# Kernel tuning notes

Hardware: AMD Instinct MI355X
Metric: run time of the kernel (lower is better)

The kernel has to match this reference:

```python
import jax, jax.numpy as jnp
import numpy as np


def setup_inputs() -> dict:
    key = jax.random.key(0)
    k_x, k_q, k_k, k_v = jax.random.split(key, 4)
    B, S, D = 8, 1024, 768
    H, DH = 12, 64
    scale = 1.0 / np.sqrt(D)
    return {
        "x": jax.random.normal(k_x, (B, S, D), dtype=jnp.float32),
        "Wq": jax.random.normal(k_q, (H, D, DH), dtype=jnp.float32) * scale,
        "Wk": jax.random.normal(k_k, (H, D, DH), dtype=jnp.float32) * scale,
        "Wv": jax.random.normal(k_v, (H, D, DH), dtype=jnp.float32) * scale,
    }


def reference(x, Wq, Wk, Wv):
    # x: [B, S, D]; Wq/Wk/Wv: [H, D, DH] (per-head Linear weights, no bias)
    B, S, D = x.shape
    H, _, DH = Wq.shape
    q = jnp.einsum("bsd,hde->bhse", x, Wq)  # [B,H,S,DH]
    k = jnp.einsum("bsd,hde->bhse", x, Wk)
    v = jnp.einsum("bsd,hde->bhse", x, Wv)
    scores = jnp.einsum("bhse,bhte->bhst", q, k) / jnp.sqrt(jnp.float32(DH))
    causal = jnp.tril(jnp.ones((S, S), dtype=bool))  # keep lower triangle
    scores = jnp.where(causal, scores, -jnp.inf)
    attn = jax.nn.softmax(scores, axis=-1)  # dropout = 0.0 -> identity
    ctx = jnp.einsum("bhst,bhte->bhse", attn, v)  # [B,H,S,DH]
    # concat heads on last dim: [B,S,H*DH]
    return ctx.transpose(0, 2, 1, 3).reshape(B, S, H * DH)
```

## Files before the change

### kernel.cpp

```cpp
#include <hip/hip_runtime.h>


#define Bq 8
#define Sq 1024
#define Dq 768
#define Hq 12
#define DHq 64

typedef _Float16 f16;
typedef f16 f16x8 __attribute__((ext_vector_type(8)));
typedef float f32x4 __attribute__((ext_vector_type(4)));

#define MFMA16(a, b, c) __builtin_amdgcn_mfma_f32_16x16x32_f16(a, b, c, 0, 0, 0)

#define QSCL 0.1803368801111244f

#if __has_builtin(__builtin_amdgcn_exp2f)
#define EXP2(x) __builtin_amdgcn_exp2f(x)
#else
#define EXP2(x) exp2f(x)
#endif

__device__ __forceinline__ void gload16(const f16* g, f16* l) {
  __builtin_amdgcn_global_load_lds(
      (const __attribute__((address_space(1))) void*)g,
      (__attribute__((address_space(3))) void*)l, 16, 0, 0);
}

__global__ __launch_bounds__(256) void cvt_x_kernel(const float* __restrict__ x,
                                                    f16* __restrict__ xh) {
  int i = blockIdx.x * 256 + threadIdx.x;
  const float4* src = reinterpret_cast<const float4*>(x) + i * 2;
  float4 a = src[0], b = src[1];
  f16x8 o;
  o[0] = (f16)a.x; o[1] = (f16)a.y; o[2] = (f16)a.z; o[3] = (f16)a.w;
  o[4] = (f16)b.x; o[5] = (f16)b.y; o[6] = (f16)b.z; o[7] = (f16)b.w;
  *reinterpret_cast<f16x8*>(xh + i * 8) = o;
}

__global__ __launch_bounds__(256) void cvt_w_kernel(const float* __restrict__ Wq,
                                                    const float* __restrict__ Wk,
                                                    const float* __restrict__ Wv,
                                                    f16* __restrict__ WT) {
  __shared__ float tile[64][65];
  const int kt = blockIdx.x, h = blockIdx.y, w = blockIdx.z;
  const float* W = (w == 0) ? Wq : (w == 1) ? Wk : Wv;
  const int t = threadIdx.x;
  const int c0 = t & 63, r4 = t >> 6;
#pragma unroll
  for (int i = 0; i < 16; i++) {
    int kr = i * 4 + r4;
    tile[kr][c0] = W[((size_t)h * Dq + kt * 64 + kr) * DHq + c0];
  }
  __syncthreads();
#pragma unroll
  for (int i = 0; i < 16; i++) {
    int e2 = i * 4 + r4;
    WT[((size_t)(w * Hq + h) * DHq + e2) * Dq + kt * 64 + c0] = (f16)tile[c0][e2];
  }
}

__global__ __launch_bounds__(256) void proj_kernel(const f16* __restrict__ xh,
                                                   const f16* __restrict__ WT,
                                                   f16* __restrict__ Q,
                                                   f16* __restrict__ K,
                                                   f16* __restrict__ Vt) {
  __shared__ __align__(1024) f16 smem[30720];

  const int mt = blockIdx.x;
  const int h = blockIdx.y;
  const int row0 = mt * 128;
  const int t = threadIdx.x;
  const int wv = t >> 6;
  const int lane = t & 63;
  const int g = lane >> 4;
  const int ql = lane & 15;
  const int wvm = wv >> 1, wvn = wv & 1;

  const int lr = lane >> 2;
  const int scg = (lane & 3) ^ ((lane >> 3) & 3);

  const f16* xsrc = xh + (size_t)row0 * Dq;
  const f16* wsrc = WT + (size_t)h * DHq * Dq;

  const f16* gA0 = xsrc + (size_t)(wv * 32 + lr) * Dq + scg * 8;
  const f16* gA1 = gA0 + (size_t)16 * Dq;
  const int n0 = wv * 48 + lr, n1 = n0 + 16, n2 = n0 + 32;
  const f16* gB0 = wsrc + ((size_t)(n0 >> 6) * Hq * DHq + (n0 & 63)) * Dq + scg * 8;
  const f16* gB1 = wsrc + ((size_t)(n1 >> 6) * Hq * DHq + (n1 & 63)) * Dq + scg * 8;
  const f16* gB2 = wsrc + ((size_t)(n2 >> 6) * Hq * DHq + (n2 & 63)) * Dq + scg * 8;

  f32x4 acc[4][6] = {};

#define PROJ_STAGE(buf)                                              \
  do {                                                               \
    f16* sA_ = smem + (buf) * 4096 + wv * 1024;                      \
    f16* sB_ = smem + 12288 + (buf) * 6144 + wv * 1536;              \
    gload16(gA0, sA_); gload16(gA1, sA_ + 512);                      \
    gload16(gB0, sB_); gload16(gB1, sB_ + 512);                      \
    gload16(gB2, sB_ + 1024);                                        \
    gA0 += 32; gA1 += 32; gB0 += 32; gB1 += 32; gB2 += 32;           \
  } while (0)

  PROJ_STAGE(0);
  PROJ_STAGE(1);

  const int rq = (g ^ ((ql >> 1) & 3)) * 8;
  const f16* rA = smem + (wvm * 64 + ql) * 32 + rq;
  const f16* rB = smem + 12288 + (wvn * 96 + ql) * 32 + rq;

#pragma unroll
  for (int step = 0; step < 24; step++) {
    if (step < 23) asm volatile("s_waitcnt vmcnt(5) lgkmcnt(0)" ::: "memory");
    else           asm volatile("s_waitcnt vmcnt(0) lgkmcnt(0)" ::: "memory");
    __builtin_amdgcn_s_barrier();
    __builtin_amdgcn_sched_barrier(0);
    if (step < 22) PROJ_STAGE((step + 2) % 3);
    const int cur = step % 3;
    f16x8 af[4], bf[6];
#pragma unroll
    for (int mf = 0; mf < 4; mf++)
      af[mf] = *reinterpret_cast<const f16x8*>(rA + cur * 4096 + mf * 512);
#pragma unroll
    for (int nf = 0; nf < 6; nf++)
      bf[nf] = *reinterpret_cast<const f16x8*>(rB + cur * 6144 + nf * 512);
    __builtin_amdgcn_s_setprio(1);
#pragma unroll
    for (int mf = 0; mf < 4; mf++)
#pragma unroll
      for (int nf = 0; nf < 6; nf++)
        acc[mf][nf] = MFMA16(af[mf], bf[nf], acc[mf][nf]);
    __builtin_amdgcn_s_setprio(0);
  }
#undef PROJ_STAGE
  __syncthreads();

  const int b = row0 >> 10;
  const int s0 = row0 & 1023;
  const size_t base_sd = ((size_t)(b * Hq + h) * Sq) * DHq;

#pragma unroll
  for (int nf = 0; nf < 6; nf++) {
    const int c = wvn * 96 + nf * 16 + ql;
    const int w = c >> 6;
    if (w < 2) {
      f16* dst = (w == 0 ? Q : K);
      const float scl = (w == 0) ? QSCL : 1.0f;
      const int e = c & 63;
#pragma unroll
      for (int mf = 0; mf < 4; mf++) {
        const int sr = wvm * 64 + mf * 16 + g * 4;
#pragma unroll
        for (int r = 0; r < 4; r++)
          dst[base_sd + (size_t)(s0 + sr + r) * DHq + e] = (f16)(acc[mf][nf][r] * scl);
      }
    }
  }

  f16* vbuf = smem;
#pragma unroll
  for (int nf = 2; nf < 6; nf++) {
    if (wvn == 1) {
      const int e = (96 + nf * 16 + ql) & 63;
#pragma unroll
      for (int mf = 0; mf < 4; mf++) {
        const int sr = wvm * 64 + mf * 16 + g * 4;
        union { f16 hh[4]; uint2 u; } z;
#pragma unroll
        for (int r = 0; r < 4; r++) z.hh[r] = (f16)acc[mf][nf][r];
        *reinterpret_cast<uint2*>(&vbuf[e * 136 + sr]) = z.u;
      }
    }
  }
  __syncthreads();
#pragma unroll
  for (int i = 0; i < 4; i++) {
    int c = t + 256 * i;
    int e = c >> 4, p = (c & 15) * 8;
    *reinterpret_cast<uint4*>(Vt + base_sd + (size_t)e * Sq + s0 + p) =
        *reinterpret_cast<const uint4*>(vbuf + e * 136 + p);
  }
}

__global__ __launch_bounds__(256) void attn_kernel(const f16* __restrict__ Q,
                                                   const f16* __restrict__ K,
                                                   const f16* __restrict__ Vt,
                                                   float* __restrict__ out) {
  __shared__ __align__(16) f16 k_lds[2][64][72];
  __shared__ __align__(16) f16 vt_lds[2][64][72];

  const int L = blockIdx.x;
  const int m = L >> 3;
  const int pr = m / Hq;
  const int bh = (L & 7) * Hq + (m % Hq);
  const int t = threadIdx.x;
  const int wv = t >> 6;
  const int lane = t & 63;
  const int g = lane >> 4;
  const int ql = lane & 15;

  const f16* Qb = Q + (size_t)bh * Sq * DHq;
  const f16* Kb = K + (size_t)bh * Sq * DHq;
  const f16* Vtb = Vt + (size_t)bh * DHq * Sq;
  const int b = bh / Hq, h = bh % Hq;

  const int r0 = t >> 3;
  const int p0 = (t & 7) * 8;

  for (int ph = 0; ph < 2; ph++) {
    const int mt = ph ? (15 - pr) : pr;
    const int q0 = mt * 64;
    const int qg = q0 + wv * 16 + ql;
    f16x8 qf0 = *reinterpret_cast<const f16x8*>(Qb + (size_t)qg * DHq + g * 8);
    f16x8 qf1 = *reinterpret_cast<const f16x8*>(Qb + (size_t)qg * DHq + 32 + g * 8);

    f32x4 o_acc[4] = {};
    float m_r = -__builtin_inff(), l_r = 0.f;

    uint4 kreg0, kreg1, vreg0, vreg1;
    kreg0 = *reinterpret_cast<const uint4*>(Kb + (size_t)r0 * DHq + p0);
    kreg1 = *reinterpret_cast<const uint4*>(Kb + (size_t)(32 + r0) * DHq + p0);
    vreg0 = *reinterpret_cast<const uint4*>(Vtb + (size_t)r0 * Sq + p0);
    vreg1 = *reinterpret_cast<const uint4*>(Vtb + (size_t)(32 + r0) * Sq + p0);
    *reinterpret_cast<uint4*>(&k_lds[0][r0][p0]) = kreg0;
    *reinterpret_cast<uint4*>(&k_lds[0][32 + r0][p0]) = kreg1;
    *reinterpret_cast<uint4*>(&vt_lds[0][r0][p0]) = vreg0;
    *reinterpret_cast<uint4*>(&vt_lds[0][32 + r0][p0]) = vreg1;
    if (mt >= 1) {
      kreg0 = *reinterpret_cast<const uint4*>(Kb + (size_t)(64 + r0) * DHq + p0);
      kreg1 = *reinterpret_cast<const uint4*>(Kb + (size_t)(96 + r0) * DHq + p0);
      vreg0 = *reinterpret_cast<const uint4*>(Vtb + (size_t)r0 * Sq + 64 + p0);
      vreg1 = *reinterpret_cast<const uint4*>(Vtb + (size_t)(32 + r0) * Sq + 64 + p0);
    }
    __syncthreads();

    int cur = 0;
    for (int kt = 0; kt <= mt; kt++) {
      f32x4 sf[4] = {};
      __builtin_amdgcn_s_setprio(1);
#pragma unroll
      for (int nt = 0; nt < 4; nt++) {
        f16x8 kf0 = *reinterpret_cast<const f16x8*>(&k_lds[cur][nt * 16 + ql][g * 8]);
        f16x8 kf1 = *reinterpret_cast<const f16x8*>(&k_lds[cur][nt * 16 + ql][32 + g * 8]);
        sf[nt] = MFMA16(kf0, qf0, sf[nt]);
        sf[nt] = MFMA16(kf1, qf1, sf[nt]);
      }
      __builtin_amdgcn_s_setprio(0);

      if (kt == mt) {
#pragma unroll
        for (int nt = 0; nt < 4; nt++)
#pragma unroll
          for (int r = 0; r < 4; r++)
            if (nt * 16 + g * 4 + r > wv * 16 + ql) sf[nt][r] = -__builtin_inff();
      }

      float rowmax = sf[0][0];
#pragma unroll
      for (int nt = 0; nt < 4; nt++)
#pragma unroll
        for (int r = 0; r < 4; r++) rowmax = fmaxf(rowmax, sf[nt][r]);
      rowmax = fmaxf(rowmax, __shfl_xor(rowmax, 16, 64));
      rowmax = fmaxf(rowmax, __shfl_xor(rowmax, 32, 64));
      float mnew = fmaxf(m_r, rowmax);
      float corr = EXP2(m_r - mnew);
      float p[4][4];
      float rs = 0.f;
#pragma unroll
      for (int nt = 0; nt < 4; nt++)
#pragma unroll
        for (int r = 0; r < 4; r++) {
          float pe = EXP2(sf[nt][r] - mnew);
          p[nt][r] = pe;
          rs += pe;
        }
      rs += __shfl_xor(rs, 16, 64);
      rs += __shfl_xor(rs, 32, 64);
      l_r = l_r * corr + rs;
      m_r = mnew;
#pragma unroll
      for (int nt = 0; nt < 4; nt++) {
        o_acc[nt][0] *= corr; o_acc[nt][1] *= corr;
        o_acc[nt][2] *= corr; o_acc[nt][3] *= corr;
      }

      uint32_t pk[4][2];
#pragma unroll
      for (int nt = 0; nt < 4; nt++) {
        union { f16 hh[2]; uint32_t u; } z0, z1;
        z0.hh[0] = (f16)p[nt][0]; z0.hh[1] = (f16)p[nt][1];
        z1.hh[0] = (f16)p[nt][2]; z1.hh[1] = (f16)p[nt][3];
        pk[nt][0] = z0.u; pk[nt][1] = z1.u;
      }
      const int srcA = ((g & 1) * 2) * 16 + ql;
      const int srcB = srcA + 16;
      const bool selhi = (g >> 1) != 0;
      f16x8 pf[2];
#pragma unroll
      for (int ks = 0; ks < 2; ks++) {
        uint32_t aA0 = (uint32_t)__shfl((int)pk[2 * ks][0], srcA, 64);
        uint32_t aA1 = (uint32_t)__shfl((int)pk[2 * ks][1], srcA, 64);
        uint32_t aB0 = (uint32_t)__shfl((int)pk[2 * ks][0], srcB, 64);
        uint32_t aB1 = (uint32_t)__shfl((int)pk[2 * ks][1], srcB, 64);
        uint32_t bA0 = (uint32_t)__shfl((int)pk[2 * ks + 1][0], srcA, 64);
        uint32_t bA1 = (uint32_t)__shfl((int)pk[2 * ks + 1][1], srcA, 64);
        uint32_t bB0 = (uint32_t)__shfl((int)pk[2 * ks + 1][0], srcB, 64);
        uint32_t bB1 = (uint32_t)__shfl((int)pk[2 * ks + 1][1], srcB, 64);
        union { uint32_t w[4]; f16x8 v; } z;
        z.w[0] = selhi ? bA0 : aA0;
        z.w[1] = selhi ? bA1 : aA1;
        z.w[2] = selhi ? bB0 : aB0;
        z.w[3] = selhi ? bB1 : aB1;
        pf[ks] = z.v;
      }

      __builtin_amdgcn_s_setprio(1);
#pragma unroll
      for (int nt = 0; nt < 4; nt++) {
        f16x8 vf0 = *reinterpret_cast<const f16x8*>(&vt_lds[cur][nt * 16 + ql][g * 8]);
        f16x8 vf1 = *reinterpret_cast<const f16x8*>(&vt_lds[cur][nt * 16 + ql][32 + g * 8]);
        o_acc[nt] = MFMA16(vf0, pf[0], o_acc[nt]);
        o_acc[nt] = MFMA16(vf1, pf[1], o_acc[nt]);
      }
      __builtin_amdgcn_s_setprio(0);

      if (kt < mt) {
        *reinterpret_cast<uint4*>(&k_lds[cur ^ 1][r0][p0]) = kreg0;
        *reinterpret_cast<uint4*>(&k_lds[cur ^ 1][32 + r0][p0]) = kreg1;
        *reinterpret_cast<uint4*>(&vt_lds[cur ^ 1][r0][p0]) = vreg0;
        *reinterpret_cast<uint4*>(&vt_lds[cur ^ 1][32 + r0][p0]) = vreg1;
        if (kt + 2 <= mt) {
          const int kv0 = (kt + 2) * 64;
          kreg0 = *reinterpret_cast<const uint4*>(Kb + (size_t)(kv0 + r0) * DHq + p0);
          kreg1 = *reinterpret_cast<const uint4*>(Kb + (size_t)(kv0 + 32 + r0) * DHq + p0);
          vreg0 = *reinterpret_cast<const uint4*>(Vtb + (size_t)r0 * Sq + kv0 + p0);
          vreg1 = *reinterpret_cast<const uint4*>(Vtb + (size_t)(32 + r0) * Sq + kv0 + p0);
        }
      }
      __syncthreads();
      cur ^= 1;
    }

    float rl = 1.0f / l_r;
    float* op = out + ((size_t)(b * Sq + qg)) * (Hq * DHq) + h * DHq;
#pragma unroll
    for (int nt = 0; nt < 4; nt++) {
      float4 st = { o_acc[nt][0] * rl, o_acc[nt][1] * rl,
                    o_acc[nt][2] * rl, o_acc[nt][3] * rl };
      *reinterpret_cast<float4*>(op + nt * 16 + g * 4) = st;
    }
  }
}

extern "C" void kernel_launch(void* const* d_in, const int* in_sizes, int n_in,
                              void* d_out, int out_size, void* d_ws, size_t ws_size,
                              hipStream_t stream) {
  const float* x = (const float*)d_in[0];
  const float* Wq = (const float*)d_in[1];
  const float* Wk = (const float*)d_in[2];
  const float* Wv = (const float*)d_in[3];
  float* out = (float*)d_out;

  const size_t off_xb = 0;
  const size_t off_wt = 12582912;
  const size_t off_q = 16121856;
  const size_t off_k = 28704768;
  const size_t off_v = 41287680;
  const size_t need = 53870592;
  if (ws_size < need) return;

  char* ws = (char*)d_ws;
  f16* xh = (f16*)(ws + off_xb);
  f16* WT = (f16*)(ws + off_wt);
  f16* Qd = (f16*)(ws + off_q);
  f16* Kd = (f16*)(ws + off_k);
  f16* Vtd = (f16*)(ws + off_v);

  cvt_x_kernel<<<3072, 256, 0, stream>>>(x, xh);
  cvt_w_kernel<<<dim3(12, 12, 3), 256, 0, stream>>>(Wq, Wk, Wv, WT);
  proj_kernel<<<dim3(64, 12), 256, 0, stream>>>(xh, WT, Qd, Kd, Vtd);
  attn_kernel<<<768, 256, 0, stream>>>(Qd, Kd, Vtd, out);
}
```

Measured before the change: 85.03 us.

## Launch one block per query tile, longest-first, with lazy softmax rescaling

The attention kernel previously had each block process a pair of complementary causal query tiles in sequence. It now launches twice as many blocks, each handling one query tile, ordered so the longest tiles are dispatched first. Online softmax now skips the max update and accumulator rescale when the new row max stays within 8 (log2 units) of the running max, and the max and sum reductions use tree form. This adds parallelism and removes serial rescale work, at the cost of more block launches and reloading Q/K per block. Skipping rescales lets exponentials reach up to 2^8, which stays within fp16 range.

```diff
diff --git a/kernel.cpp b/kernel.cpp
--- a/kernel.cpp
+++ b/kernel.cpp
@@ -190,9 +190,9 @@
   __shared__ __align__(16) f16 vt_lds[2][64][72];
 
   const int L = blockIdx.x;
-  const int m = L >> 3;
-  const int pr = m / Hq;
-  const int bh = (L & 7) * Hq + (m % Hq);
+  const int i = L >> 3;
+  const int bh = (L & 7) * Hq + (i % Hq);
+  const int mt = 15 - (i / Hq);
   const int t = threadIdx.x;
   const int wv = t >> 6;
   const int lane = t & 63;
@@ -207,148 +207,150 @@
   const int r0 = t >> 3;
   const int p0 = (t & 7) * 8;
 
-  for (int ph = 0; ph < 2; ph++) {
-    const int mt = ph ? (15 - pr) : pr;
-    const int q0 = mt * 64;
-    const int qg = q0 + wv * 16 + ql;
-    f16x8 qf0 = *reinterpret_cast<const f16x8*>(Qb + (size_t)qg * DHq + g * 8);
-    f16x8 qf1 = *reinterpret_cast<const f16x8*>(Qb + (size_t)qg * DHq + 32 + g * 8);
-
-    f32x4 o_acc[4] = {};
-    float m_r = -__builtin_inff(), l_r = 0.f;
-
-    uint4 kreg0, kreg1, vreg0, vreg1;
-    kreg0 = *reinterpret_cast<const uint4*>(Kb + (size_t)r0 * DHq + p0);
-    kreg1 = *reinterpret_cast<const uint4*>(Kb + (size_t)(32 + r0) * DHq + p0);
-    vreg0 = *reinterpret_cast<const uint4*>(Vtb + (size_t)r0 * Sq + p0);
-    vreg1 = *reinterpret_cast<const uint4*>(Vtb + (size_t)(32 + r0) * Sq + p0);
-    *reinterpret_cast<uint4*>(&k_lds[0][r0][p0]) = kreg0;
-    *reinterpret_cast<uint4*>(&k_lds[0][32 + r0][p0]) = kreg1;
-    *reinterpret_cast<uint4*>(&vt_lds[0][r0][p0]) = vreg0;
-    *reinterpret_cast<uint4*>(&vt_lds[0][32 + r0][p0]) = vreg1;
-    if (mt >= 1) {
-      kreg0 = *reinterpret_cast<const uint4*>(Kb + (size_t)(64 + r0) * DHq + p0);
-      kreg1 = *reinterpret_cast<const uint4*>(Kb + (size_t)(96 + r0) * DHq + p0);
-      vreg0 = *reinterpret_cast<const uint4*>(Vtb + (size_t)r0 * Sq + 64 + p0);
-      vreg1 = *reinterpret_cast<const uint4*>(Vtb + (size_t)(32 + r0) * Sq + 64 + p0);
-    }
-    __syncthreads();
-
-    int cur = 0;
-    for (int kt = 0; kt <= mt; kt++) {
-      f32x4 sf[4] = {};
-      __builtin_amdgcn_s_setprio(1);
-#pragma unroll
-      for (int nt = 0; nt < 4; nt++) {
-        f16x8 kf0 = *reinterpret_cast<const f16x8*>(&k_lds[cur][nt * 16 + ql][g * 8]);
-        f16x8 kf1 = *reinterpret_cast<const f16x8*>(&k_lds[cur][nt * 16 + ql][32 + g * 8]);
-        sf[nt] = MFMA16(kf0, qf0, sf[nt]);
-        sf[nt] = MFMA16(kf1, qf1, sf[nt]);
-      }
-      __builtin_amdgcn_s_setprio(0);
-
-      if (kt == mt) {
-#pragma unroll
-        for (int nt = 0; nt < 4; nt++)
-#pragma unroll
-          for (int r = 0; r < 4; r++)
-            if (nt * 16 + g * 4 + r > wv * 16 + ql) sf[nt][r] = -__builtin_inff();
-      }
-
-      float rowmax = sf[0][0];
+  const int q0 = mt * 64;
+  const int qg = q0 + wv * 16 + ql;
+  f16x8 qf0 = *reinterpret_cast<const f16x8*>(Qb + (size_t)qg * DHq + g * 8);
+  f16x8 qf1 = *reinterpret_cast<const f16x8*>(Qb + (size_t)qg * DHq + 32 + g * 8);
+
+  f32x4 o_acc[4] = {};
+  float m_r = -__builtin_inff(), l_r = 0.f;
+
+  uint4 kreg0, kreg1, vreg0, vreg1;
+  kreg0 = *reinterpret_cast<const uint4*>(Kb + (size_t)r0 * DHq + p0);
+  kreg1 = *reinterpret_cast<const uint4*>(Kb + (size_t)(32 + r0) * DHq + p0);
+  vreg0 = *reinterpret_cast<const uint4*>(Vtb + (size_t)r0 * Sq + p0);
+  vreg1 = *reinterpret_cast<const uint4*>(Vtb + (size_t)(32 + r0) * Sq + p0);
+  *reinterpret_cast<uint4*>(&k_lds[0][r0][p0]) = kreg0;
+  *reinterpret_cast<uint4*>(&k_lds[0][32 + r0][p0]) = kreg1;
+  *reinterpret_cast<uint4*>(&vt_lds[0][r0][p0]) = vreg0;
+  *reinterpret_cast<uint4*>(&vt_lds[0][32 + r0][p0]) = vreg1;
+  if (mt >= 1) {
+    kreg0 = *reinterpret_cast<const uint4*>(Kb + (size_t)(64 + r0) * DHq + p0);
+    kreg1 = *reinterpret_cast<const uint4*>(Kb + (size_t)(96 + r0) * DHq + p0);
+    vreg0 = *reinterpret_cast<const uint4*>(Vtb + (size_t)r0 * Sq + 64 + p0);
+    vreg1 = *reinterpret_cast<const uint4*>(Vtb + (size_t)(32 + r0) * Sq + 64 + p0);
+  }
+  __syncthreads();
+
+  int cur = 0;
+  for (int kt = 0; kt <= mt; kt++) {
+    f32x4 sf[4] = {};
+    __builtin_amdgcn_s_setprio(1);
+#pragma unroll
+    for (int nt = 0; nt < 4; nt++) {
+      f16x8 kf0 = *reinterpret_cast<const f16x8*>(&k_lds[cur][nt * 16 + ql][g * 8]);
+      f16x8 kf1 = *reinterpret_cast<const f16x8*>(&k_lds[cur][nt * 16 + ql][32 + g * 8]);
+      sf[nt] = MFMA16(kf0, qf0, sf[nt]);
+      sf[nt] = MFMA16(kf1, qf1, sf[nt]);
+    }
+    __builtin_amdgcn_s_setprio(0);
+
+    if (kt == mt) {
 #pragma unroll
       for (int nt = 0; nt < 4; nt++)
 #pragma unroll
-        for (int r = 0; r < 4; r++) rowmax = fmaxf(rowmax, sf[nt][r]);
-      rowmax = fmaxf(rowmax, __shfl_xor(rowmax, 16, 64));
-      rowmax = fmaxf(rowmax, __shfl_xor(rowmax, 32, 64));
+        for (int r = 0; r < 4; r++)
+          if (nt * 16 + g * 4 + r > wv * 16 + ql) sf[nt][r] = -__builtin_inff();
+    }
+
+    float t0 = fmaxf(fmaxf(sf[0][0], sf[0][1]), fmaxf(sf[0][2], sf[0][3]));
+    float t1 = fmaxf(fmaxf(sf[1][0], sf[1][1]), fmaxf(sf[1][2], sf[1][3]));
+    float t2 = fmaxf(fmaxf(sf[2][0], sf[2][1]), fmaxf(sf[2][2], sf[2][3]));
+    float t3 = fmaxf(fmaxf(sf[3][0], sf[3][1]), fmaxf(sf[3][2], sf[3][3]));
+    float rowmax = fmaxf(fmaxf(t0, t1), fmaxf(t2, t3));
+    rowmax = fmaxf(rowmax, __shfl_xor(rowmax, 16, 64));
+    rowmax = fmaxf(rowmax, __shfl_xor(rowmax, 32, 64));
+
+    if (!__all(rowmax <= m_r + 8.f)) {
       float mnew = fmaxf(m_r, rowmax);
       float corr = EXP2(m_r - mnew);
-      float p[4][4];
-      float rs = 0.f;
-#pragma unroll
-      for (int nt = 0; nt < 4; nt++)
-#pragma unroll
-        for (int r = 0; r < 4; r++) {
-          float pe = EXP2(sf[nt][r] - mnew);
-          p[nt][r] = pe;
-          rs += pe;
-        }
-      rs += __shfl_xor(rs, 16, 64);
-      rs += __shfl_xor(rs, 32, 64);
-      l_r = l_r * corr + rs;
-      m_r = mnew;
+      l_r *= corr;
 #pragma unroll
       for (int nt = 0; nt < 4; nt++) {
         o_acc[nt][0] *= corr; o_acc[nt][1] *= corr;
         o_acc[nt][2] *= corr; o_acc[nt][3] *= corr;
       }
-
-      uint32_t pk[4][2];
-#pragma unroll
-      for (int nt = 0; nt < 4; nt++) {
-        union { f16 hh[2]; uint32_t u; } z0, z1;
-        z0.hh[0] = (f16)p[nt][0]; z0.hh[1] = (f16)p[nt][1];
-        z1.hh[0] = (f16)p[nt][2]; z1.hh[1] = (f16)p[nt][3];
-        pk[nt][0] = z0.u; pk[nt][1] = z1.u;
+      m_r = mnew;
+    }
+
+    float p[4][4];
+#pragma unroll
+    for (int nt = 0; nt < 4; nt++)
+#pragma unroll
+      for (int r = 0; r < 4; r++) p[nt][r] = EXP2(sf[nt][r] - m_r);
+    float s0 = (p[0][0] + p[0][1]) + (p[0][2] + p[0][3]);
+    float s1 = (p[1][0] + p[1][1]) + (p[1][2] + p[1][3]);
+    float s2 = (p[2][0] + p[2][1]) + (p[2][2] + p[2][3]);
+    float s3 = (p[3][0] + p[3][1]) + (p[3][2] + p[3][3]);
+    float rs = (s0 + s1) + (s2 + s3);
+    rs += __shfl_xor(rs, 16, 64);
+    rs += __shfl_xor(rs, 32, 64);
+    l_r += rs;
+
+    uint32_t pk[4][2];
+#pragma unroll
+    for (int nt = 0; nt < 4; nt++) {
+      union { f16 hh[2]; uint32_t u; } z0, z1;
+      z0.hh[0] = (f16)p[nt][0]; z0.hh[1] = (f16)p[nt][1];
+      z1.hh[0] = (f16)p[nt][2]; z1.hh[1] = (f16)p[nt][3];
+      pk[nt][0] = z0.u; pk[nt][1] = z1.u;
+    }
+    const int srcA = ((g & 1) * 2) * 16 + ql;
+    const int srcB = srcA + 16;
+    const bool selhi = (g >> 1) != 0;
+    f16x8 pf[2];
+#pragma unroll
+    for (int ks = 0; ks < 2; ks++) {
+      uint32_t aA0 = (uint32_t)__shfl((int)pk[2 * ks][0], srcA, 64);
+      uint32_t aA1 = (uint32_t)__shfl((int)pk[2 * ks][1], srcA, 64);
+      uint32_t aB0 = (uint32_t)__shfl((int)pk[2 * ks][0], srcB, 64);
+      uint32_t aB1 = (uint32_t)__shfl((int)pk[2 * ks][1], srcB, 64);
+      uint32_t bA0 = (uint32_t)__shfl((int)pk[2 * ks + 1][0], srcA, 64);
+      uint32_t bA1 = (uint32_t)__shfl((int)pk[2 * ks + 1][1], srcA, 64);
+      uint32_t bB0 = (uint32_t)__shfl((int)pk[2 * ks + 1][0], srcB, 64);
+      uint32_t bB1 = (uint32_t)__shfl((int)pk[2 * ks + 1][1], srcB, 64);
+      union { uint32_t w[4]; f16x8 v; } z;
+      z.w[0] = selhi ? bA0 : aA0;
+      z.w[1] = selhi ? bA1 : aA1;
+      z.w[2] = selhi ? bB0 : aB0;
+      z.w[3] = selhi ? bB1 : aB1;
+      pf[ks] = z.v;
+    }
+
+    __builtin_amdgcn_s_setprio(1);
+#pragma unroll
+    for (int nt = 0; nt < 4; nt++) {
+      f16x8 vf0 = *reinterpret_cast<const f16x8*>(&vt_lds[cur][nt * 16 + ql][g * 8]);
+      f16x8 vf1 = *reinterpret_cast<const f16x8*>(&vt_lds[cur][nt * 16 + ql][32 + g * 8]);
+      o_acc[nt] = MFMA16(vf0, pf[0], o_acc[nt]);
+      o_acc[nt] = MFMA16(vf1, pf[1], o_acc[nt]);
+    }
+    __builtin_amdgcn_s_setprio(0);
+
+    if (kt < mt) {
+      *reinterpret_cast<uint4*>(&k_lds[cur ^ 1][r0][p0]) = kreg0;
+      *reinterpret_cast<uint4*>(&k_lds[cur ^ 1][32 + r0][p0]) = kreg1;
+      *reinterpret_cast<uint4*>(&vt_lds[cur ^ 1][r0][p0]) = vreg0;
+      *reinterpret_cast<uint4*>(&vt_lds[cur ^ 1][32 + r0][p0]) = vreg1;
+      if (kt + 2 <= mt) {
+        const int kv0 = (kt + 2) * 64;
+        kreg0 = *reinterpret_cast<const uint4*>(Kb + (size_t)(kv0 + r0) * DHq + p0);
+        kreg1 = *reinterpret_cast<const uint4*>(Kb + (size_t)(kv0 + 32 + r0) * DHq + p0);
+        vreg0 = *reinterpret_cast<const uint4*>(Vtb + (size_t)r0 * Sq + kv0 + p0);
+        vreg1 = *reinterpret_cast<const uint4*>(Vtb + (size_t)(32 + r0) * Sq + kv0 + p0);
       }
-      const int srcA = ((g & 1) * 2) * 16 + ql;
-      const int srcB = srcA + 16;
-      const bool selhi = (g >> 1) != 0;
-      f16x8 pf[2];
-#pragma unroll
-      for (int ks = 0; ks < 2; ks++) {
-        uint32_t aA0 = (uint32_t)__shfl((int)pk[2 * ks][0], srcA, 64);
-        uint32_t aA1 = (uint32_t)__shfl((int)pk[2 * ks][1], srcA, 64);
-        uint32_t aB0 = (uint32_t)__shfl((int)pk[2 * ks][0], srcB, 64);
-        uint32_t aB1 = (uint32_t)__shfl((int)pk[2 * ks][1], srcB, 64);
-        uint32_t bA0 = (uint32_t)__shfl((int)pk[2 * ks + 1][0], srcA, 64);
-        uint32_t bA1 = (uint32_t)__shfl((int)pk[2 * ks + 1][1], srcA, 64);
-        uint32_t bB0 = (uint32_t)__shfl((int)pk[2 * ks + 1][0], srcB, 64);
-        uint32_t bB1 = (uint32_t)__shfl((int)pk[2 * ks + 1][1], srcB, 64);
-        union { uint32_t w[4]; f16x8 v; } z;
-        z.w[0] = selhi ? bA0 : aA0;
-        z.w[1] = selhi ? bA1 : aA1;
-        z.w[2] = selhi ? bB0 : aB0;
-        z.w[3] = selhi ? bB1 : aB1;
-        pf[ks] = z.v;
-      }
-
-      __builtin_amdgcn_s_setprio(1);
-#pragma unroll
-      for (int nt = 0; nt < 4; nt++) {
-        f16x8 vf0 = *reinterpret_cast<const f16x8*>(&vt_lds[cur][nt * 16 + ql][g * 8]);
-        f16x8 vf1 = *reinterpret_cast<const f16x8*>(&vt_lds[cur][nt * 16 + ql][32 + g * 8]);
-        o_acc[nt] = MFMA16(vf0, pf[0], o_acc[nt]);
-        o_acc[nt] = MFMA16(vf1, pf[1], o_acc[nt]);
-      }
-      __builtin_amdgcn_s_setprio(0);
-
-      if (kt < mt) {
-        *reinterpret_cast<uint4*>(&k_lds[cur ^ 1][r0][p0]) = kreg0;
-        *reinterpret_cast<uint4*>(&k_lds[cur ^ 1][32 + r0][p0]) = kreg1;
-        *reinterpret_cast<uint4*>(&vt_lds[cur ^ 1][r0][p0]) = vreg0;
-        *reinterpret_cast<uint4*>(&vt_lds[cur ^ 1][32 + r0][p0]) = vreg1;
-        if (kt + 2 <= mt) {
-          const int kv0 = (kt + 2) * 64;
-          kreg0 = *reinterpret_cast<const uint4*>(Kb + (size_t)(kv0 + r0) * DHq + p0);
-          kreg1 = *reinterpret_cast<const uint4*>(Kb + (size_t)(kv0 + 32 + r0) * DHq + p0);
-          vreg0 = *reinterpret_cast<const uint4*>(Vtb + (size_t)r0 * Sq + kv0 + p0);
-          vreg1 = *reinterpret_cast<const uint4*>(Vtb + (size_t)(32 + r0) * Sq + kv0 + p0);
-        }
-      }
-      __syncthreads();
-      cur ^= 1;
-    }
-
-    float rl = 1.0f / l_r;
-    float* op = out + ((size_t)(b * Sq + qg)) * (Hq * DHq) + h * DHq;
-#pragma unroll
-    for (int nt = 0; nt < 4; nt++) {
-      float4 st = { o_acc[nt][0] * rl, o_acc[nt][1] * rl,
-                    o_acc[nt][2] * rl, o_acc[nt][3] * rl };
-      *reinterpret_cast<float4*>(op + nt * 16 + g * 4) = st;
-    }
+    }
+    __syncthreads();
+    cur ^= 1;
+  }
+
+  float rl = 1.0f / l_r;
+  float* op = out + ((size_t)(b * Sq + qg)) * (Hq * DHq) + h * DHq;
+#pragma unroll
+  for (int nt = 0; nt < 4; nt++) {
+    float4 st = { o_acc[nt][0] * rl, o_acc[nt][1] * rl,
+                  o_acc[nt][2] * rl, o_acc[nt][3] * rl };
+    *reinterpret_cast<float4*>(op + nt * 16 + g * 4) = st;
   }
 }
 
@@ -379,5 +381,5 @@
   cvt_x_kernel<<<3072, 256, 0, stream>>>(x, xh);
   cvt_w_kernel<<<dim3(12, 12, 3), 256, 0, stream>>>(Wq, Wk, Wv, WT);
   proj_kernel<<<dim3(64, 12), 256, 0, stream>>>(xh, WT, Qd, Kd, Vtd);
-  attn_kernel<<<768, 256, 0, stream>>>(Qd, Kd, Vtd, out);
-}
+  attn_kernel<<<1536, 256, 0, stream>>>(Qd, Kd, Vtd, out);
+}
```

Result: no change. 86.35 us (+1.5%).
